# Kernel optimization log

Measured on AMD Instinct MI355X. Metric: run time of the kernel, lower is better.

## Reference

```python
import jax, jax.numpy as jnp
import numpy as np

B, M, S, N, L = 8, 10, 200, 2048, 128
BETA = 0.01
EPS = 1e-6


def quat_to_rot(q):
    # q: (..., 4) = (w, x, y, z)
    q = q / jnp.linalg.norm(q, axis=-1, keepdims=True)
    w, x, y, z = q[..., 0], q[..., 1], q[..., 2], q[..., 3]
    r0 = jnp.stack([1 - 2 * (y * y + z * z), 2 * (x * y - w * z), 2 * (x * z + w * y)], -1)
    r1 = jnp.stack([2 * (x * y + w * z), 1 - 2 * (x * x + z * z), 2 * (y * z - w * x)], -1)
    r2 = jnp.stack([2 * (x * z - w * y), 2 * (y * z + w * x), 1 - 2 * (x * x + y * y)], -1)
    return jnp.stack([r0, r1, r2], -2)  # (..., 3, 3)


def fexp(x, p):
    # signed power, clamped away from 0 for numerical safety
    return jnp.sign(x) * jnp.maximum(jnp.abs(x), EPS) ** p


def setup_inputs() -> dict:
    key = jax.random.key(0)
    ks = jax.random.split(key, 11)
    ipts = jax.random.normal(ks[0], (B, N, 3), jnp.float32)
    translations = 0.3 * jax.random.normal(ks[1], (B, M, 3), jnp.float32)
    rotations = jax.random.normal(ks[2], (B, M, 4), jnp.float32)
    size = 0.05 + 0.55 * jax.random.uniform(ks[3], (B, M, 3), dtype=jnp.float32)
    shape_e = 0.2 + 1.4 * jax.random.uniform(ks[4], (B, M, 2), dtype=jnp.float32)
    deformations = 0.9 * (jax.random.uniform(ks[5], (B, M, 2), dtype=jnp.float32) - 0.5)
    probs = jax.nn.sigmoid(jax.random.normal(ks[6], (B, M), jnp.float32))
    etas = (jax.random.uniform(ks[7], (B, M, S), dtype=jnp.float32) - 0.5) * jnp.pi
    omegas = (jax.random.uniform(ks[8], (B, M, S), dtype=jnp.float32) - 0.5) * 2.0 * jnp.pi
    mu = jax.random.normal(ks[9], (B, L), jnp.float32)
    logvar = 0.1 * jax.random.normal(ks[10], (B, L), jnp.float32)
    return {"ipts": ipts, "translations": translations, "rotations": rotations,
            "size": size, "shape_e": shape_e, "deformations": deformations,
            "probs": probs, "etas": etas, "omegas": omegas, "mu": mu, "logvar": logvar}


def reference(ipts, translations, rotations, size, shape_e, deformations,
              probs, etas, omegas, mu, logvar):
    # ---- transform points into primitive-centric frames: (B,N,M,3) ----
    R = quat_to_rot(rotations)                              # (B,M,3,3)
    Xc = ipts[:, :, None, :] - translations[:, None, :, :]  # (B,N,M,3)
    Xt = jnp.einsum('bmij,bnmj->bnmi', R, Xc)               # (B,N,M,3)

    # ---- sample points on superquadric surfaces: (B,M,S,3) ----
    e1, e2 = shape_e[..., 0:1], shape_e[..., 1:2]           # (B,M,1)
    ce, se = jnp.cos(etas), jnp.sin(etas)
    co, so = jnp.cos(omegas), jnp.sin(omegas)
    px = size[..., 0:1] * fexp(ce, e1) * fexp(co, e2)
    py = size[..., 1:2] * fexp(ce, e1) * fexp(so, e2)
    pz = size[..., 2:3] * fexp(se, e1)
    pts = jnp.stack([px, py, pz], -1)                       # (B,M,S,3)

    # ---- linear tapering deformation along z ----
    a3 = size[:, :, None, 2:3]                              # (B,M,1,1)
    f = deformations[:, :, None, :] * pts[..., 2:3] / a3 + 1.0  # (B,M,S,2)
    pts = jnp.concatenate([pts[..., :2] * f, pts[..., 2:3]], -1)

    # ---- pairwise squared distances (B,M,S,N) ----
    diff = pts[:, :, :, None, :] - jnp.transpose(Xt, (0, 2, 1, 3))[:, :, None, :, :]
    dist = jnp.sum(diff * diff, -1)                         # (B,M,S,N)

    # ---- pcl -> prim loss (expectation over existence probabilities) ----
    V = jnp.transpose(jnp.min(dist, axis=2), (0, 2, 1))     # (B,N,M)
    order = jnp.argsort(V, axis=-1)
    Vs = jnp.take_along_axis(V, order, -1)
    ps = jnp.take_along_axis(jnp.broadcast_to(probs[:, None, :], V.shape), order, -1)
    neg = jnp.cumprod(1.0 - ps, axis=-1)
    neg = jnp.concatenate([jnp.ones_like(neg[..., :1]), neg[..., :-1]], -1)
    Fs = ps * neg                                            # prob m-th closest existing
    pcl_to_prim = jnp.mean(jnp.sum(Fs * Vs, -1))

    # ---- prim -> pcl loss ----
    d_mp = jnp.mean(jnp.min(dist, axis=-1), axis=-1)         # (B,M)
    prim_to_pcl = jnp.mean(jnp.sum(probs * d_mp, -1))

    prims = pcl_to_prim + prim_to_pcl
    regs = jnp.float32(0.0)  # regularizer_terms = {} -> zero regularization
    kld = jnp.mean(-0.5 * jnp.sum(1.0 + logvar - mu * mu - jnp.exp(logvar), -1))
    total = prims + regs + BETA * kld
    return total, prims, regs, kld
```

## Files before the change

### kernel.cpp

```cpp
#include <hip/hip_runtime.h>
#include <math.h>

#define B_ 8
#define M_ 10
#define S_ 200
#define PADS_ 208
#define N_ 2048
#define L_ 128
#define BETA_ 0.01f
#define EPS_ 1e-6f
#define INF_U 0x7F7F7F7Fu
#define SENT_ 5.0e18f

#define NT_ 128
#define TILES_ (N_ / NT_)
#define DIST_BLOCKS (B_ * M_ * TILES_)
#define VS_BLOCKS ((B_ * N_) / 256)
#define MID_BLOCKS (VS_BLOCKS + B_*M_)

__device__ __forceinline__ float fexp_(float x, float p) {
    float s = (x > 0.f) ? 1.f : ((x < 0.f) ? -1.f : 0.f);
    return s * powf(fmaxf(fabsf(x), EPS_), p);
}

__global__ __launch_bounds__(256) void dist_k(
    const float* __restrict__ ipts,  const float* __restrict__ trans,
    const float* __restrict__ rot,   const float* __restrict__ psize,
    const float* __restrict__ shp,   const float* __restrict__ def,
    const float* __restrict__ etas,  const float* __restrict__ omegas,
    float* __restrict__ vpart, float* __restrict__ spart)
{
    __shared__ float4 sPts[PADS_];
    __shared__ float4 sXt[NT_];
    __shared__ unsigned int sMinS[PADS_];
    __shared__ float sV[NT_];
    __shared__ float sR[9];

    const int t    = threadIdx.x;
    const int tile = blockIdx.x % TILES_;
    const int bm   = blockIdx.x / TILES_;
    const int b    = bm / M_;
    const int lane = t & 63, wave = t >> 6;

    if (t == 0) {
        float w = rot[bm*4+0], x = rot[bm*4+1], y = rot[bm*4+2], z = rot[bm*4+3];
        float inv = 1.f / sqrtf(w*w + x*x + y*y + z*z);
        w *= inv; x *= inv; y *= inv; z *= inv;
        sR[0] = 1.f - 2.f*(y*y + z*z); sR[1] = 2.f*(x*y - w*z);       sR[2] = 2.f*(x*z + w*y);
        sR[3] = 2.f*(x*y + w*z);       sR[4] = 1.f - 2.f*(x*x + z*z); sR[5] = 2.f*(y*z - w*x);
        sR[6] = 2.f*(x*z - w*y);       sR[7] = 2.f*(y*z + w*x);       sR[8] = 1.f - 2.f*(x*x + y*y);
    }
    if (t < PADS_) {
        sMinS[t] = INF_U;
        if (t < S_) {
            float a1 = psize[bm*3+0], a2 = psize[bm*3+1], a3 = psize[bm*3+2];
            float e1 = shp[bm*2+0],  e2 = shp[bm*2+1];
            float d0 = def[bm*2+0],  d1 = def[bm*2+1];
            float eta = etas[bm*S_+t], om = omegas[bm*S_+t];
            float ce = cosf(eta), se = sinf(eta);
            float co = cosf(om),  so = sinf(om);
            float fce = fexp_(ce, e1), fse = fexp_(se, e1);
            float fco = fexp_(co, e2), fso = fexp_(so, e2);
            float px = a1 * fce * fco;
            float py = a2 * fce * fso;
            float pz = a3 * fse;
            float fr = pz / a3;
            px *= d0*fr + 1.f;
            py *= d1*fr + 1.f;
            sPts[t] = make_float4(px, py, pz, px*px + py*py + pz*pz);
        } else {
            sPts[t] = make_float4(SENT_, SENT_, SENT_, 3.f*SENT_*SENT_);
        }
    }
    __syncthreads();

    if (t < NT_) {
        int n = tile*NT_ + t;
        const float* ip = ipts + (size_t)(b*N_ + n)*3;
        float cx = ip[0] - trans[bm*3+0];
        float cy = ip[1] - trans[bm*3+1];
        float cz = ip[2] - trans[bm*3+2];
        float X0 = sR[0]*cx + sR[1]*cy + sR[2]*cz;
        float X1 = sR[3]*cx + sR[4]*cy + sR[5]*cz;
        float X2 = sR[6]*cx + sR[7]*cy + sR[8]*cz;
        sXt[t] = make_float4(-2.f*X0, -2.f*X1, -2.f*X2, X0*X0 + X1*X1 + X2*X2);
    }
    __syncthreads();

    const int sg = lane & 15;
    const int ng = wave*4 + (lane >> 4);

    float4 A[8];
    #pragma unroll
    for (int j = 0; j < 8; ++j) A[j] = sXt[ng*8 + j];

    float vmin[8];
    #pragma unroll
    for (int j = 0; j < 8; ++j) vmin[j] = 3.4e38f;

    #pragma unroll 4
    for (int k = 0; k < 13; ++k) {
        float4 p = sPts[k*16 + sg];
        float dm = 3.4e38f;
        #pragma unroll
        for (int j = 0; j < 8; ++j) {
            float d = fmaf(p.x, A[j].x,
                      fmaf(p.y, A[j].y,
                      fmaf(p.z, A[j].z, p.w + A[j].w)));
            vmin[j] = fminf(vmin[j], d);
            dm = fminf(dm, d);
        }
        dm = fminf(dm, __shfl_xor(dm, 16));
        dm = fminf(dm, __shfl_xor(dm, 32));
        if (lane < 16) atomicMin(&sMinS[k*16 + sg], __float_as_uint(dm));
    }

    #pragma unroll
    for (int j = 0; j < 8; ++j) {
        float v = vmin[j];
        #pragma unroll
        for (int o = 1; o < 16; o <<= 1) v = fminf(v, __shfl_xor(v, o));
        vmin[j] = v;
    }
    if (sg == 0) {
        #pragma unroll
        for (int j = 0; j < 8; ++j) sV[ng*8 + j] = vmin[j];
    }
    __syncthreads();

    if (t < NT_) vpart[bm*N_ + tile*NT_ + t] = sV[t];
    if (t < S_)  spart[(size_t)(bm*TILES_ + tile)*S_ + t] = __uint_as_float(sMinS[t]);
}

__global__ __launch_bounds__(256) void mid_k(const float* __restrict__ vpart,
                                             const float* __restrict__ spart,
                                             const float* __restrict__ probs,
                                             float* __restrict__ pclpart,
                                             float* __restrict__ dmpW)
{
    __shared__ float sSum[4];
    int t = threadIdx.x, lane = t & 63, wave = t >> 6;

    if (blockIdx.x < VS_BLOCKS) {
        int g = blockIdx.x*256 + t;
        int b = g / N_, n = g % N_;
        float V[M_], P[M_];
        #pragma unroll
        for (int m = 0; m < M_; ++m) {
            V[m] = vpart[(b*M_ + m)*N_ + n];
            P[m] = probs[b*M_ + m];
        }
        #pragma unroll
        for (int i = 0; i < M_-1; ++i)
            #pragma unroll
            for (int j = 0; j < M_-1-i; ++j)
                if (V[j] > V[j+1]) {
                    float tv = V[j]; V[j] = V[j+1]; V[j+1] = tv;
                    float tp = P[j]; P[j] = P[j+1]; P[j+1] = tp;
                }
        float cum = 1.f, sum = 0.f;
        #pragma unroll
        for (int i = 0; i < M_; ++i) { sum += P[i] * cum * V[i]; cum *= (1.f - P[i]); }

        #pragma unroll
        for (int o = 1; o < 64; o <<= 1) sum += __shfl_xor(sum, o);
        if (lane == 0) sSum[wave] = sum;
        __syncthreads();
        if (t == 0) pclpart[blockIdx.x] = sSum[0] + sSum[1] + sSum[2] + sSum[3];
    } else {
        int bm = blockIdx.x - VS_BLOCKS;
        float v = 0.f;
        if (t < S_) {
            const float* sp = spart + (size_t)bm*TILES_*S_ + t;
            float mn = 3.4e38f;
            #pragma unroll
            for (int tl = 0; tl < TILES_; ++tl) mn = fminf(mn, sp[tl*S_]);
            v = mn;
        }
        #pragma unroll
        for (int o = 1; o < 64; o <<= 1) v += __shfl_xor(v, o);
        if (lane == 0) sSum[wave] = v;
        __syncthreads();
        if (t == 0) dmpW[bm] = (sSum[0] + sSum[1] + sSum[2] + sSum[3]) * probs[bm];
    }
}

__global__ __launch_bounds__(256) void final_k(const float* __restrict__ pclpart,
                                               const float* __restrict__ dmpW,
                                               const float* __restrict__ mu,
                                               const float* __restrict__ logvar,
                                               float* __restrict__ out)
{
    int t = threadIdx.x, lane = t & 63, wave = t >> 6;
    float s0 = (t < VS_BLOCKS) ? pclpart[t] : 0.f;
    float s1 = (t < B_*M_)     ? dmpW[t]    : 0.f;
    float s2 = 0.f;
    for (int i = t; i < B_*L_; i += 256) {
        float muv = mu[i], lv = logvar[i];
        s2 += -0.5f * (1.f + lv - muv*muv - expf(lv));
    }
    #pragma unroll
    for (int o = 1; o < 64; o <<= 1) {
        s0 += __shfl_xor(s0, o);
        s1 += __shfl_xor(s1, o);
        s2 += __shfl_xor(s2, o);
    }
    __shared__ float sRed[12];
    if (lane == 0) { sRed[wave] = s0; sRed[4+wave] = s1; sRed[8+wave] = s2; }
    __syncthreads();
    if (t == 0) {
        float S0 = sRed[0] + sRed[1] + sRed[2] + sRed[3];
        float S1 = sRed[4] + sRed[5] + sRed[6] + sRed[7];
        float S2 = sRed[8] + sRed[9] + sRed[10] + sRed[11];
        float pcl_to_prim = S0 / (float)(B_ * N_);
        float prim_to_pcl = S1 / (float)(B_ * S_);
        float kld = S2 / (float)B_;
        float prims = pcl_to_prim + prim_to_pcl;
        out[0] = prims + BETA_ * kld;
        out[1] = prims;
        out[2] = 0.f;
        out[3] = kld;
    }
}

extern "C" void kernel_launch(void* const* d_in, const int* in_sizes, int n_in,
                              void* d_out, int out_size, void* d_ws, size_t ws_size,
                              hipStream_t stream) {
    const float* ipts    = (const float*)d_in[0];
    const float* trans   = (const float*)d_in[1];
    const float* rot     = (const float*)d_in[2];
    const float* psize   = (const float*)d_in[3];
    const float* shp     = (const float*)d_in[4];
    const float* def     = (const float*)d_in[5];
    const float* probs   = (const float*)d_in[6];
    const float* etas    = (const float*)d_in[7];
    const float* omegas  = (const float*)d_in[8];
    const float* mu      = (const float*)d_in[9];
    const float* logvar  = (const float*)d_in[10];
    float* out = (float*)d_out;

    char* ws = (char*)d_ws;
    float* vpart   = (float*)(ws);
    float* spart   = (float*)(ws + 655360);
    float* pclpart = (float*)(ws + 1679360);
    float* dmpW    = (float*)(ws + 1679616);

    dist_k<<<DIST_BLOCKS, 256, 0, stream>>>(ipts, trans, rot, psize, shp, def,
                                            etas, omegas, vpart, spart);
    mid_k<<<MID_BLOCKS, 256, 0, stream>>>(vpart, spart, probs, pclpart, dmpW);
    final_k<<<1, 256, 0, stream>>>(pclpart, dmpW, mu, logvar, out);
}
```

Before: 26.80 us.

## Fuse final reduction into mid kernel via atomics and double point tile size

Drops the third kernel launch: the mid kernel now accumulates the scaled partial losses and the KLD term straight into the output with atomicAdd, and the first kernel zeroes the output. The point tile grows from 128 to 256, so every thread keeps 16 points in registers and the number of distance blocks halves. Per-sample minimums are gathered in registers and reduced once after the loop, the lane reductions use DPP moves, and vpart is written with float4 stores. Fast-math sin, cos and pow replace the precise versions, which changes accuracy and makes float summation order non-deterministic, and the larger register footprint may lower occupancy.

```diff
diff --git a/kernel.cpp b/kernel.cpp
--- a/kernel.cpp
+++ b/kernel.cpp
@@ -12,15 +12,18 @@
 #define INF_U 0x7F7F7F7Fu
 #define SENT_ 5.0e18f
 
-#define NT_ 128
+#define NT_ 256
 #define TILES_ (N_ / NT_)
 #define DIST_BLOCKS (B_ * M_ * TILES_)
 #define VS_BLOCKS ((B_ * N_) / 256)
-#define MID_BLOCKS (VS_BLOCKS + B_*M_)
+#define MID_BLOCKS (VS_BLOCKS + B_*M_ + 1)
+
+#define DPPMIN_(v, ctrl) \
+    v = fminf(v, __int_as_float(__builtin_amdgcn_mov_dpp(__float_as_int(v), ctrl, 0xf, 0xf, true)))
 
 __device__ __forceinline__ float fexp_(float x, float p) {
     float s = (x > 0.f) ? 1.f : ((x < 0.f) ? -1.f : 0.f);
-    return s * powf(fmaxf(fabsf(x), EPS_), p);
+    return s * __powf(fmaxf(fabsf(x), EPS_), p);
 }
 
 __global__ __launch_bounds__(256) void dist_k(
@@ -28,12 +31,12 @@
     const float* __restrict__ rot,   const float* __restrict__ psize,
     const float* __restrict__ shp,   const float* __restrict__ def,
     const float* __restrict__ etas,  const float* __restrict__ omegas,
-    float* __restrict__ vpart, float* __restrict__ spart)
+    float* __restrict__ vpart, float* __restrict__ spart,
+    float* __restrict__ out)
 {
     __shared__ float4 sPts[PADS_];
     __shared__ float4 sXt[NT_];
     __shared__ unsigned int sMinS[PADS_];
-    __shared__ float sV[NT_];
     __shared__ float sR[9];
 
     const int t    = threadIdx.x;
@@ -41,6 +44,8 @@
     const int bm   = blockIdx.x / TILES_;
     const int b    = bm / M_;
     const int lane = t & 63, wave = t >> 6;
+
+    if (blockIdx.x == 0 && t < 4) out[t] = 0.f;
 
     if (t == 0) {
         float w = rot[bm*4+0], x = rot[bm*4+1], y = rot[bm*4+2], z = rot[bm*4+3];
@@ -57,8 +62,8 @@
             float e1 = shp[bm*2+0],  e2 = shp[bm*2+1];
             float d0 = def[bm*2+0],  d1 = def[bm*2+1];
             float eta = etas[bm*S_+t], om = omegas[bm*S_+t];
-            float ce = cosf(eta), se = sinf(eta);
-            float co = cosf(om),  so = sinf(om);
+            float ce = __cosf(eta), se = __sinf(eta);
+            float co = __cosf(om),  so = __sinf(om);
             float fce = fexp_(ce, e1), fse = fexp_(se, e1);
             float fco = fexp_(co, e2), fso = fexp_(so, e2);
             float px = a1 * fce * fco;
@@ -74,7 +79,7 @@
     }
     __syncthreads();
 
-    if (t < NT_) {
+    {
         int n = tile*NT_ + t;
         const float* ip = ipts + (size_t)(b*N_ + n)*3;
         float cx = ip[0] - trans[bm*3+0];
@@ -90,53 +95,70 @@
     const int sg = lane & 15;
     const int ng = wave*4 + (lane >> 4);
 
-    float4 A[8];
-    #pragma unroll
-    for (int j = 0; j < 8; ++j) A[j] = sXt[ng*8 + j];
-
-    float vmin[8];
-    #pragma unroll
-    for (int j = 0; j < 8; ++j) vmin[j] = 3.4e38f;
-
-    #pragma unroll 4
+    float4 A[16];
+    #pragma unroll
+    for (int j = 0; j < 16; ++j) A[j] = sXt[ng*16 + j];
+
+    float vmin[16];
+    #pragma unroll
+    for (int j = 0; j < 16; ++j) vmin[j] = 3.4e38f;
+
+    float sm[13];
+
+    #pragma unroll
     for (int k = 0; k < 13; ++k) {
         float4 p = sPts[k*16 + sg];
-        float dm = 3.4e38f;
-        #pragma unroll
-        for (int j = 0; j < 8; ++j) {
-            float d = fmaf(p.x, A[j].x,
-                      fmaf(p.y, A[j].y,
-                      fmaf(p.z, A[j].z, p.w + A[j].w)));
-            vmin[j] = fminf(vmin[j], d);
-            dm = fminf(dm, d);
-        }
-        dm = fminf(dm, __shfl_xor(dm, 16));
-        dm = fminf(dm, __shfl_xor(dm, 32));
-        if (lane < 16) atomicMin(&sMinS[k*16 + sg], __float_as_uint(dm));
-    }
-
-    #pragma unroll
-    for (int j = 0; j < 8; ++j) {
+        float d[16];
+        #pragma unroll
+        for (int j = 0; j < 16; ++j) {
+            d[j] = fmaf(p.x, A[j].x,
+                   fmaf(p.y, A[j].y,
+                   fmaf(p.z, A[j].z, p.w + A[j].w)));
+            vmin[j] = fminf(vmin[j], d[j]);
+        }
+        #pragma unroll
+        for (int st = 8; st >= 1; st >>= 1)
+            #pragma unroll
+            for (int j = 0; j < st; ++j)
+                d[j] = fminf(d[j], d[j + st]);
+        sm[k] = d[0];
+    }
+
+    #pragma unroll
+    for (int k = 0; k < 13; ++k) {
+        float v = sm[k];
+        v = fminf(v, __shfl_xor(v, 16));
+        v = fminf(v, __shfl_xor(v, 32));
+        if (lane < 16) atomicMin(&sMinS[k*16 + sg], __float_as_uint(v));
+    }
+
+    #pragma unroll
+    for (int j = 0; j < 16; ++j) {
         float v = vmin[j];
-        #pragma unroll
-        for (int o = 1; o < 16; o <<= 1) v = fminf(v, __shfl_xor(v, o));
+        DPPMIN_(v, 0xB1);
+        DPPMIN_(v, 0x4E);
+        DPPMIN_(v, 0x141);
+        DPPMIN_(v, 0x140);
         vmin[j] = v;
     }
     if (sg == 0) {
-        #pragma unroll
-        for (int j = 0; j < 8; ++j) sV[ng*8 + j] = vmin[j];
-    }
+        float* vp = vpart + bm*N_ + tile*NT_ + ng*16;
+        #pragma unroll
+        for (int q = 0; q < 4; ++q)
+            *reinterpret_cast<float4*>(vp + q*4) =
+                make_float4(vmin[q*4+0], vmin[q*4+1], vmin[q*4+2], vmin[q*4+3]);
+    }
+
     __syncthreads();
-
-    if (t < NT_) vpart[bm*N_ + tile*NT_ + t] = sV[t];
-    if (t < S_)  spart[(size_t)(bm*TILES_ + tile)*S_ + t] = __uint_as_float(sMinS[t]);
+    if (t < S_) spart[(size_t)(bm*TILES_ + tile)*S_ + t] = __uint_as_float(sMinS[t]);
 }
 
 __global__ __launch_bounds__(256) void mid_k(const float* __restrict__ vpart,
                                              const float* __restrict__ spart,
                                              const float* __restrict__ probs,
-                                             float* __restrict__ pclpart,
-                                             float* __restrict__ dmpW)
+                                             const float* __restrict__ mu,
+                                             const float* __restrict__ logvar,
+                                             float* __restrict__ out)
 {
     __shared__ float sSum[4];
     int t = threadIdx.x, lane = t & 63, wave = t >> 6;
@@ -166,8 +188,12 @@
         for (int o = 1; o < 64; o <<= 1) sum += __shfl_xor(sum, o);
         if (lane == 0) sSum[wave] = sum;
         __syncthreads();
-        if (t == 0) pclpart[blockIdx.x] = sSum[0] + sSum[1] + sSum[2] + sSum[3];
-    } else {
+        if (t == 0) {
+            float v = (sSum[0] + sSum[1] + sSum[2] + sSum[3]) / (float)(B_ * N_);
+            atomicAdd(&out[0], v);
+            atomicAdd(&out[1], v);
+        }
+    } else if (blockIdx.x < VS_BLOCKS + B_*M_) {
         int bm = blockIdx.x - VS_BLOCKS;
         float v = 0.f;
         if (t < S_) {
@@ -181,45 +207,27 @@
         for (int o = 1; o < 64; o <<= 1) v += __shfl_xor(v, o);
         if (lane == 0) sSum[wave] = v;
         __syncthreads();
-        if (t == 0) dmpW[bm] = (sSum[0] + sSum[1] + sSum[2] + sSum[3]) * probs[bm];
-    }
-}
-
-__global__ __launch_bounds__(256) void final_k(const float* __restrict__ pclpart,
-                                               const float* __restrict__ dmpW,
-                                               const float* __restrict__ mu,
-                                               const float* __restrict__ logvar,
-                                               float* __restrict__ out)
-{
-    int t = threadIdx.x, lane = t & 63, wave = t >> 6;
-    float s0 = (t < VS_BLOCKS) ? pclpart[t] : 0.f;
-    float s1 = (t < B_*M_)     ? dmpW[t]    : 0.f;
-    float s2 = 0.f;
-    for (int i = t; i < B_*L_; i += 256) {
-        float muv = mu[i], lv = logvar[i];
-        s2 += -0.5f * (1.f + lv - muv*muv - expf(lv));
-    }
-    #pragma unroll
-    for (int o = 1; o < 64; o <<= 1) {
-        s0 += __shfl_xor(s0, o);
-        s1 += __shfl_xor(s1, o);
-        s2 += __shfl_xor(s2, o);
-    }
-    __shared__ float sRed[12];
-    if (lane == 0) { sRed[wave] = s0; sRed[4+wave] = s1; sRed[8+wave] = s2; }
-    __syncthreads();
-    if (t == 0) {
-        float S0 = sRed[0] + sRed[1] + sRed[2] + sRed[3];
-        float S1 = sRed[4] + sRed[5] + sRed[6] + sRed[7];
-        float S2 = sRed[8] + sRed[9] + sRed[10] + sRed[11];
-        float pcl_to_prim = S0 / (float)(B_ * N_);
-        float prim_to_pcl = S1 / (float)(B_ * S_);
-        float kld = S2 / (float)B_;
-        float prims = pcl_to_prim + prim_to_pcl;
-        out[0] = prims + BETA_ * kld;
-        out[1] = prims;
-        out[2] = 0.f;
-        out[3] = kld;
+        if (t == 0) {
+            float s = (sSum[0] + sSum[1] + sSum[2] + sSum[3]) * probs[bm]
+                      / (float)(B_ * S_);
+            atomicAdd(&out[0], s);
+            atomicAdd(&out[1], s);
+        }
+    } else {
+        float s2 = 0.f;
+        for (int i = t; i < B_*L_; i += 256) {
+            float muv = mu[i], lv = logvar[i];
+            s2 += -0.5f * (1.f + lv - muv*muv - expf(lv));
+        }
+        #pragma unroll
+        for (int o = 1; o < 64; o <<= 1) s2 += __shfl_xor(s2, o);
+        if (lane == 0) sSum[wave] = s2;
+        __syncthreads();
+        if (t == 0) {
+            float kld = (sSum[0] + sSum[1] + sSum[2] + sSum[3]) / (float)B_;
+            atomicAdd(&out[0], BETA_ * kld);
+            atomicAdd(&out[3], kld);
+        }
     }
 }
 
@@ -240,13 +248,10 @@
     float* out = (float*)d_out;
 
     char* ws = (char*)d_ws;
-    float* vpart   = (float*)(ws);
-    float* spart   = (float*)(ws + 655360);
-    float* pclpart = (float*)(ws + 1679360);
-    float* dmpW    = (float*)(ws + 1679616);
+    float* vpart = (float*)(ws);
+    float* spart = (float*)(ws + 655360);
 
     dist_k<<<DIST_BLOCKS, 256, 0, stream>>>(ipts, trans, rot, psize, shp, def,
-                                            etas, omegas, vpart, spart);
-    mid_k<<<MID_BLOCKS, 256, 0, stream>>>(vpart, spart, probs, pclpart, dmpW);
-    final_k<<<1, 256, 0, stream>>>(pclpart, dmpW, mu, logvar, out);
-}
+                                            etas, omegas, vpart, spart, out);
+    mid_k<<<MID_BLOCKS, 256, 0, stream>>>(vpart, spart, probs, mu, logvar, out);
+}
```

Result: slower. 30.90 us (+15.3%).
